# Kernel tuning notes

Measured on AMD Instinct MI355X. Metric: run time of the kernel, lower is better.

Reference implementation:

```python
import jax, jax.numpy as jnp
import numpy as np

EMBED = 1024
NUM_EXPERTS = 8
ACTIVE = 2
HIDDEN = 4 * EMBED


def setup_inputs() -> dict:
    key = jax.random.key(0)
    ks = jax.random.split(key, 7)
    B, T = 4, 1024
    s1 = 1.0 / np.sqrt(EMBED)
    s2 = 1.0 / np.sqrt(HIDDEN)
    return {
        "x": jax.random.normal(ks[0], (B, T, EMBED), dtype=jnp.float32),
        # stacked expert weights, layout [in, out] (torch Linear applies x @ W.T + b)
        "W1": jax.random.uniform(ks[1], (NUM_EXPERTS, EMBED, HIDDEN), jnp.float32, -s1, s1),
        "b1": jax.random.uniform(ks[2], (NUM_EXPERTS, HIDDEN), jnp.float32, -s1, s1),
        "W2": jax.random.uniform(ks[3], (NUM_EXPERTS, HIDDEN, EMBED), jnp.float32, -s2, s2),
        "b2": jax.random.uniform(ks[4], (NUM_EXPERTS, EMBED), jnp.float32, -s2, s2),
        "Wr": jax.random.uniform(ks[5], (EMBED, NUM_EXPERTS), jnp.float32, -s1, s1),
        "br": jax.random.uniform(ks[6], (NUM_EXPERTS,), jnp.float32, -s1, s1),
    }


def reference(x, W1, b1, W2, b2, Wr, br):
    # ---- router (TopkRouter) ----
    scores = x @ Wr + br                                  # [B,T,E]
    topk_scores, indices = jax.lax.top_k(scores, ACTIVE)  # [B,T,K]
    # mask = zeros scattered with topk scores at topk positions (others stay 0),
    # then softmax over ALL experts (faithful to the reference's quirky softmax).
    one_hot = jax.nn.one_hot(indices, NUM_EXPERTS, dtype=scores.dtype)  # [B,T,K,E]
    mask = jnp.einsum('btke,btk->bte', one_hot, topk_scores)            # [B,T,E]
    router_output = jax.nn.softmax(mask, axis=-1)                       # [B,T,E]

    # ---- dense all-experts FFN (Expert): relu(x@W1+b1)@W2+b2 per expert ----
    h = jax.nn.relu(jnp.einsum('btd,edh->bteh', x, W1) + b1)            # [B,T,E,H]
    expert_outputs = jnp.einsum('bteh,ehd->bted', h, W2) + b2           # [B,T,E,D]

    # ---- weighted combine ----
    return jnp.einsum('bte,bted->btd', router_output, expert_outputs)   # [B,T,D]
```

## Files before the change

### kernel.cpp

```cpp
#include <hip/hip_runtime.h>
#include <hip/hip_bf16.h>
#include <cstdint>
#include <cstddef>

#define EMBED  1024
#define NEXP   8
#define HIDDEN 4096
#define TOKENS 4096

typedef __attribute__((ext_vector_type(8))) short bf16x8;
typedef __attribute__((ext_vector_type(4))) float f32x4;
using bf16 = __hip_bfloat16;

__device__ __forceinline__ void gload_lds16(const void* g, void* l) {
    __builtin_amdgcn_global_load_lds((const __attribute__((address_space(1))) void*)g,
                                     (__attribute__((address_space(3))) void*)l,
                                     16, 0, 0);
}

__device__ __forceinline__ int swzB(int b) { return b ^ (((b >> 7) & 7) << 4); }

__global__ void cvt_kernel(const float* __restrict__ in, bf16* __restrict__ out, size_t n) {
    size_t i = ((size_t)blockIdx.x * blockDim.x + threadIdx.x) * 4;
    if (i + 3 < n) {
        float4 v = *(const float4*)(in + i);
        out[i + 0] = __float2bfloat16(v.x);
        out[i + 1] = __float2bfloat16(v.y);
        out[i + 2] = __float2bfloat16(v.z);
        out[i + 3] = __float2bfloat16(v.w);
    }
}

__global__ void transpose_cvt(const float* __restrict__ in, bf16* __restrict__ out,
                              int K, int N, size_t in_estride, size_t out_eoff, int ldo) {
    const int e = blockIdx.z;
    const float* ine = in + (size_t)e * in_estride;
    bf16* oute = out + (size_t)e * out_eoff;
    __shared__ float tile[32][33];
    const int n0 = blockIdx.x * 32, k0 = blockIdx.y * 32;
    const int tx = threadIdx.x, ty = threadIdx.y;
    #pragma unroll
    for (int i = ty; i < 32; i += 8)
        tile[i][tx] = ine[(size_t)(k0 + i) * N + n0 + tx];
    __syncthreads();
    #pragma unroll
    for (int i = ty; i < 32; i += 8)
        oute[(size_t)(n0 + i) * ldo + k0 + tx] = __float2bfloat16(tile[tx][i]);
}

__global__ void router_kernel(const float* __restrict__ x, const float* __restrict__ Wr,
                              const float* __restrict__ br, float* __restrict__ w) {
    const int t = blockIdx.x;
    const int lane = threadIdx.x;
    const float* xt = x + (size_t)t * EMBED;
    float s[NEXP];
    #pragma unroll
    for (int e = 0; e < NEXP; e++) s[e] = 0.f;
    for (int k = lane; k < EMBED; k += 64) {
        const float xv = xt[k];
        const float* wrk = Wr + (size_t)k * NEXP;
        #pragma unroll
        for (int e = 0; e < NEXP; e++) s[e] = fmaf(xv, wrk[e], s[e]);
    }
    #pragma unroll
    for (int e = 0; e < NEXP; e++) {
        #pragma unroll
        for (int off = 32; off >= 1; off >>= 1)
            s[e] += __shfl_xor(s[e], off);
    }
    if (lane == 0) {
        float sc[NEXP];
        #pragma unroll
        for (int e = 0; e < NEXP; e++) sc[e] = s[e] + br[e];
        int i1 = 0; float m1 = sc[0];
        #pragma unroll
        for (int e = 1; e < NEXP; e++) if (sc[e] > m1) { m1 = sc[e]; i1 = e; }
        int i2 = -1; float m2 = -1e30f;
        #pragma unroll
        for (int e = 0; e < NEXP; e++) if (e != i1 && sc[e] > m2) { m2 = sc[e]; i2 = e; }
        const float mx = fmaxf(m1, 0.f);
        const float denom = 6.f * expf(0.f - mx) + expf(m1 - mx) + expf(m2 - mx);
        #pragma unroll
        for (int e = 0; e < NEXP; e++) {
            float v = (e == i1) ? m1 : ((e == i2) ? m2 : 0.f);
            w[(size_t)t * NEXP + e] = expf(v - mx) / denom;
        }
    }
}

__global__ __launch_bounds__(256) void reduce_kernel(const float* __restrict__ p,
                                                     const float* __restrict__ rw,
                                                     const float* __restrict__ b2,
                                                     float* __restrict__ out) {
    const int row = blockIdx.x;
    const int c4 = threadIdx.x * 4;
    const size_t S = (size_t)TOKENS * EMBED;
    const float* pr = p + (size_t)row * EMBED + c4;
    float4 v0 = *(const float4*)(pr);
    float4 v1 = *(const float4*)(pr + S);
    float4 v2 = *(const float4*)(pr + 2 * S);
    float4 v3 = *(const float4*)(pr + 3 * S);
    float4 v;
    v.x = v0.x + v1.x + v2.x + v3.x;
    v.y = v0.y + v1.y + v2.y + v3.y;
    v.z = v0.z + v1.z + v2.z + v3.z;
    v.w = v0.w + v1.w + v2.w + v3.w;
    const float* wrow = rw + (size_t)row * NEXP;
    #pragma unroll
    for (int e = 0; e < NEXP; e++) {
        const float we = wrow[e];
        float4 bb = *(const float4*)(b2 + (size_t)e * EMBED + c4);
        v.x = fmaf(we, bb.x, v.x);
        v.y = fmaf(we, bb.y, v.y);
        v.z = fmaf(we, bb.z, v.z);
        v.w = fmaf(we, bb.w, v.w);
    }
    *(float4*)(out + (size_t)row * EMBED + c4) = v;
}

#define BARX()  { __builtin_amdgcn_sched_barrier(0); __builtin_amdgcn_s_barrier(); __builtin_amdgcn_sched_barrier(0); }
#define LGKM0() { asm volatile("s_waitcnt lgkmcnt(0)" ::: "memory"); __builtin_amdgcn_sched_barrier(0); }

#define KOFF(T, estride) ((size_t)((T) & 63) * 64 + (size_t)((T) >> 6) * (estride))

#define PIPE_PREAMBLE(Abase, Bbase, lda, ldb)                                        \
    __shared__ __align__(16) bf16 As[2][2][128 * 64];                                \
    __shared__ __align__(16) bf16 Bs[2][2][128 * 64];                                \
    const int tid = threadIdx.x;                                                     \
    const int lane = tid & 63, wid = tid >> 6;                                       \
    const int mhalf = wid >> 2, wB = wid & 3;                                        \
    const int nhalf = wB >> 1, nsub = wB & 1;                                        \
    const int wv_r = mhalf * 128, wv_c = wB * 64;                                    \
    f32x4 acc[8][4] = {};                                                            \
    int rowloc[2], colel[2];                                                         \
    _Pragma("unroll")                                                                \
    for (int j = 0; j < 2; j++) {                                                    \
        int bs = swzB(tid * 16 + j * 8192);                                          \
        rowloc[j] = bs >> 7; colel[j] = (bs & 127) >> 1;                             \
    }                                                                                \
    const bf16* pA0 = (Abase) + (size_t)(brow + rowloc[0]) * (lda) + colel[0];       \
    const bf16* pA1 = (Abase) + (size_t)(brow + rowloc[1]) * (lda) + colel[1];       \
    const bf16* pB0 = (Bbase) + (size_t)(bcol + rowloc[0]) * (ldb) + colel[0];       \
    const bf16* pB1 = (Bbase) + (size_t)(bcol + rowloc[1]) * (ldb) + colel[1];       \
    const int fr = lane & 15, kb0 = (lane >> 4) * 16;                                \
    const int xm = (fr & 7) << 4;                                                    \
    const int baA0 = (fr * 128 + kb0) ^ xm, baA1 = (fr * 128 + kb0 + 64) ^ xm;       \
    const int brB = (nsub * 64 + fr) * 128;                                          \
    const int baB0 = (brB + kb0) ^ xm, baB1 = (brB + kb0 + 64) ^ xm;

#define STAGE_A(bi, h, koff, lda)                                                    \
    do {                                                                             \
        gload_lds16(pA0 + (size_t)(h) * 128 * (lda) + (koff), &As[bi][h][tid * 8]);  \
        gload_lds16(pA1 + (size_t)(h) * 128 * (lda) + (koff), &As[bi][h][tid * 8 + 4096]); \
    } while (0)
#define STAGE_B(bi, h, koff, ldb)                                                    \
    do {                                                                             \
        gload_lds16(pB0 + (size_t)(h) * 128 * (ldb) + (koff), &Bs[bi][h][tid * 8]);  \
        gload_lds16(pB1 + (size_t)(h) * 128 * (ldb) + (koff), &Bs[bi][h][tid * 8 + 4096]); \
    } while (0)

#define MFMA_Q(mh, nh)                                                               \
    __builtin_amdgcn_s_setprio(1);                                                   \
    _Pragma("unroll")                                                                \
    for (int mm = 0; mm < 4; mm++)                                                   \
        _Pragma("unroll")                                                            \
        for (int nn = 0; nn < 2; nn++) {                                             \
            acc[(mh)*4+mm][(nh)*2+nn] = __builtin_amdgcn_mfma_f32_16x16x32_bf16(     \
                a[(mh)*4+mm][0], b[(nh)*2+nn][0], acc[(mh)*4+mm][(nh)*2+nn], 0,0,0); \
            acc[(mh)*4+mm][(nh)*2+nn] = __builtin_amdgcn_mfma_f32_16x16x32_bf16(     \
                a[(mh)*4+mm][1], b[(nh)*2+nn][1], acc[(mh)*4+mm][(nh)*2+nn], 0,0,0); \
        }                                                                            \
    __builtin_amdgcn_s_setprio(0);

#define PIPE_KLOOP(NT, lda, ldb, eA, eB)                                             \
    STAGE_A(0, 0, 0, lda); STAGE_A(0, 1, 0, lda);                                    \
    STAGE_B(0, 0, 0, ldb); STAGE_B(0, 1, 0, ldb);                                    \
    STAGE_A(1, 0, 64, lda); STAGE_A(1, 1, 64, lda);                                  \
    STAGE_B(1, 0, 64, ldb); STAGE_B(1, 1, 64, ldb);                                  \
    asm volatile("s_waitcnt vmcnt(8)" ::: "memory");                                 \
    BARX();                                                                          \
    for (int t = 0; t < (NT); ++t) {                                                 \
        const int bi = t & 1;                                                        \
        const bool st = (t + 2) < (NT);                                              \
        const size_t koffA = KOFF(t + 2, eA);                                        \
        const size_t koffB = KOFF(t + 2, eB);                                        \
        const char* Ah = (const char*)&As[bi][mhalf][0];                             \
        const char* Bh = (const char*)&Bs[bi][nhalf][0];                             \
        bf16x8 a[8][2], b[4][2];                                                     \
                                        \
        _Pragma("unroll")                                                            \
        for (int m = 0; m < 4; m++) {                                                \
            a[m][0] = *(const bf16x8*)(Ah + baA0 + m * 2048);                        \
            a[m][1] = *(const bf16x8*)(Ah + baA1 + m * 2048);                        \
        }                                                                            \
        _Pragma("unroll")                                                            \
        for (int n = 0; n < 2; n++) {                                                \
            b[n][0] = *(const bf16x8*)(Bh + baB0 + n * 2048);                        \
            b[n][1] = *(const bf16x8*)(Bh + baB1 + n * 2048);                        \
        }                                                                            \
        BARX(); LGKM0();                                                             \
        MFMA_Q(0, 0)                                                                 \
                                                   \
        _Pragma("unroll")                                                            \
        for (int n = 2; n < 4; n++) {                                                \
            b[n][0] = *(const bf16x8*)(Bh + baB0 + n * 2048);                        \
            b[n][1] = *(const bf16x8*)(Bh + baB1 + n * 2048);                        \
        }                                                                            \
        BARX(); LGKM0();                                                             \
        MFMA_Q(0, 1)                                                                 \
        BARX();                                                                      \
                                     \
        _Pragma("unroll")                                                            \
        for (int m = 4; m < 8; m++) {                                                \
            a[m][0] = *(const bf16x8*)(Ah + baA0 + m * 2048);                        \
            a[m][1] = *(const bf16x8*)(Ah + baA1 + m * 2048);                        \
        }                                                                            \
        if (st) { STAGE_B(bi, 0, koffB, ldb); STAGE_B(bi, 1, koffB, ldb); }          \
        BARX(); LGKM0();                                                             \
        MFMA_Q(1, 0)                                                                 \
        BARX();                                                                      \
                       \
        if (st) { STAGE_A(bi, 0, koffA, lda); STAGE_A(bi, 1, koffA, lda); }          \
        MFMA_Q(1, 1)                                                                 \
        if (st) { asm volatile("s_waitcnt vmcnt(8)" ::: "memory"); }                 \
        else    { asm volatile("s_waitcnt vmcnt(0)" ::: "memory"); }                 \
        BARX();                                                                      \
    }

__global__ __launch_bounds__(512, 2) void gemm1(const bf16* __restrict__ A,
                                                const bf16* __restrict__ Bt,
                                                const float* __restrict__ b1,
                                                const float* __restrict__ rw,
                                                bf16* __restrict__ H) {
    const int e = blockIdx.z;
    const int brow = blockIdx.y * 256;
    const int bcol = blockIdx.x * 256;
    const bf16* Be = Bt + (size_t)e * HIDDEN * EMBED;
    bf16* He = H + (size_t)e * TOKENS * HIDDEN;

    PIPE_PREAMBLE(A, Be, EMBED, EMBED)
    PIPE_KLOOP(16, EMBED, EMBED, (size_t)0, (size_t)0)

    #pragma unroll
    for (int n = 0; n < 4; n++) {
        const int col = bcol + wv_c + n * 16 + fr;
        const float bias = b1[e * HIDDEN + col];
        #pragma unroll
        for (int m = 0; m < 8; m++) {
            const int rowb = brow + wv_r + m * 16 + (lane >> 4) * 4;
            #pragma unroll
            for (int j = 0; j < 4; j++) {
                const int row = rowb + j;
                float v = acc[m][n][j] + bias;
                v = fmaxf(v, 0.f) * rw[(size_t)row * NEXP + e];
                He[(size_t)row * HIDDEN + col] = __float2bfloat16(v);
            }
        }
    }
}

__global__ __launch_bounds__(512, 2) void gemm2(const bf16* __restrict__ A,
                                                const bf16* __restrict__ Bt,
                                                float* __restrict__ partials) {
    const int kc = blockIdx.z;
    const int brow = blockIdx.y * 256;
    const int bcol = blockIdx.x * 256;
    const size_t eA = (size_t)TOKENS * HIDDEN;
    const size_t eB = (size_t)EMBED * HIDDEN;
    const bf16* Ae = A + (size_t)(kc * 2) * eA;
    const bf16* Be = Bt + (size_t)(kc * 2) * eB;
    float* pout = partials + (size_t)kc * TOKENS * EMBED;

    PIPE_PREAMBLE(Ae, Be, HIDDEN, HIDDEN)
    PIPE_KLOOP(128, HIDDEN, HIDDEN, eA, eB)

    #pragma unroll
    for (int n = 0; n < 4; n++) {
        const int col = bcol + wv_c + n * 16 + fr;
        #pragma unroll
        for (int m = 0; m < 8; m++) {
            const int rowb = brow + wv_r + m * 16 + (lane >> 4) * 4;
            #pragma unroll
            for (int j = 0; j < 4; j++) {
                const int row = rowb + j;
                pout[(size_t)row * EMBED + col] = acc[m][n][j];
            }
        }
    }
}

extern "C" void kernel_launch(void* const* d_in, const int* in_sizes, int n_in,
                              void* d_out, int out_size, void* d_ws, size_t ws_size,
                              hipStream_t stream) {
    const float* x  = (const float*)d_in[0];
    const float* W1 = (const float*)d_in[1];
    const float* b1 = (const float*)d_in[2];
    const float* W2 = (const float*)d_in[3];
    const float* b2 = (const float*)d_in[4];
    const float* Wr = (const float*)d_in[5];
    const float* br = (const float*)d_in[6];
    float* out = (float*)d_out;

    uint8_t* ws = (uint8_t*)d_ws;
    size_t off = 0;
    auto walloc = [&](size_t bytes) -> void* {
        void* p = ws + off;
        off += (bytes + 255) & ~(size_t)255;
        return p;
    };
    float* rw  = (float*)walloc((size_t)TOKENS * NEXP * 4);
    bf16* xb   = (bf16*)walloc((size_t)TOKENS * EMBED * 2);
    bf16* w1t  = (bf16*)walloc((size_t)NEXP * HIDDEN * EMBED * 2);
    bf16* w2t  = (bf16*)walloc((size_t)NEXP * EMBED * HIDDEN * 2);
    bf16* hbuf = (bf16*)walloc((size_t)NEXP * TOKENS * HIDDEN * 2);
    float* partials = (float*)w1t;

    cvt_kernel<<<4096, 256, 0, stream>>>(x, xb, (size_t)TOKENS * EMBED);

    dim3 tb(32, 8);
    transpose_cvt<<<dim3(HIDDEN / 32, EMBED / 32, NEXP), tb, 0, stream>>>(
        W1, w1t, EMBED, HIDDEN, (size_t)EMBED * HIDDEN, (size_t)HIDDEN * EMBED, EMBED);
    transpose_cvt<<<dim3(EMBED / 32, HIDDEN / 32, NEXP), tb, 0, stream>>>(
        W2, w2t, HIDDEN, EMBED, (size_t)HIDDEN * EMBED, (size_t)EMBED * HIDDEN, HIDDEN);

    router_kernel<<<TOKENS, 64, 0, stream>>>(x, Wr, br, rw);

    gemm1<<<dim3(HIDDEN / 256, TOKENS / 256, NEXP), 512, 0, stream>>>(xb, w1t, b1, rw, hbuf);
    gemm2<<<dim3(EMBED / 256, TOKENS / 256, 4), 512, 0, stream>>>(hbuf, w2t, partials);
    reduce_kernel<<<TOKENS, 256, 0, stream>>>(partials, rw, b2, out);
}
```

Before: 813.2 us.

## Make gemm1 persistent over eight row tiles with a continuous K pipeline

gemm1 now launches 256 blocks, each of which walks 8 consecutive 256-row tiles in a single 128-step pipelined loop. The loop keeps prefetching the next tile's A and B across tile boundaries, writes each tile's epilogue inline, and then zeroes the accumulators. Router weights and biases are staged into LDS and registers once per block, and the loop-body reads are factored into macros. The aim is to remove per-tile pipeline fill/drain and launch overhead. In exchange there are fewer blocks (256 on a large GPU), which risks under-occupancy, and the epilogue stores stall the pipeline.

```diff
diff --git a/kernel.cpp b/kernel.cpp
--- a/kernel.cpp
+++ b/kernel.cpp
@@ -172,6 +172,32 @@
         }                                                                            \
     __builtin_amdgcn_s_setprio(0);
 
+#define PH1_READS()                                                                  \
+    _Pragma("unroll")                                                                \
+    for (int m = 0; m < 4; m++) {                                                    \
+        a[m][0] = *(const bf16x8*)(Ah + baA0 + m * 2048);                            \
+        a[m][1] = *(const bf16x8*)(Ah + baA1 + m * 2048);                            \
+    }                                                                                \
+    _Pragma("unroll")                                                                \
+    for (int n = 0; n < 2; n++) {                                                    \
+        b[n][0] = *(const bf16x8*)(Bh + baB0 + n * 2048);                            \
+        b[n][1] = *(const bf16x8*)(Bh + baB1 + n * 2048);                            \
+    }
+
+#define PH2_READS()                                                                  \
+    _Pragma("unroll")                                                                \
+    for (int n = 2; n < 4; n++) {                                                    \
+        b[n][0] = *(const bf16x8*)(Bh + baB0 + n * 2048);                            \
+        b[n][1] = *(const bf16x8*)(Bh + baB1 + n * 2048);                            \
+    }
+
+#define PH3_READS()                                                                  \
+    _Pragma("unroll")                                                                \
+    for (int m = 4; m < 8; m++) {                                                    \
+        a[m][0] = *(const bf16x8*)(Ah + baA0 + m * 2048);                            \
+        a[m][1] = *(const bf16x8*)(Ah + baA1 + m * 2048);                            \
+    }
+
 #define PIPE_KLOOP(NT, lda, ldb, eA, eB)                                             \
     STAGE_A(0, 0, 0, lda); STAGE_A(0, 1, 0, lda);                                    \
     STAGE_B(0, 0, 0, ldb); STAGE_B(0, 1, 0, ldb);                                    \
@@ -187,39 +213,18 @@
         const char* Ah = (const char*)&As[bi][mhalf][0];                             \
         const char* Bh = (const char*)&Bs[bi][nhalf][0];                             \
         bf16x8 a[8][2], b[4][2];                                                     \
-                                        \
-        _Pragma("unroll")                                                            \
-        for (int m = 0; m < 4; m++) {                                                \
-            a[m][0] = *(const bf16x8*)(Ah + baA0 + m * 2048);                        \
-            a[m][1] = *(const bf16x8*)(Ah + baA1 + m * 2048);                        \
-        }                                                                            \
-        _Pragma("unroll")                                                            \
-        for (int n = 0; n < 2; n++) {                                                \
-            b[n][0] = *(const bf16x8*)(Bh + baB0 + n * 2048);                        \
-            b[n][1] = *(const bf16x8*)(Bh + baB1 + n * 2048);                        \
-        }                                                                            \
+        PH1_READS()                                                                  \
         BARX(); LGKM0();                                                             \
         MFMA_Q(0, 0)                                                                 \
-                                                   \
-        _Pragma("unroll")                                                            \
-        for (int n = 2; n < 4; n++) {                                                \
-            b[n][0] = *(const bf16x8*)(Bh + baB0 + n * 2048);                        \
-            b[n][1] = *(const bf16x8*)(Bh + baB1 + n * 2048);                        \
-        }                                                                            \
+        PH2_READS()                                                                  \
         BARX(); LGKM0();                                                             \
         MFMA_Q(0, 1)                                                                 \
         BARX();                                                                      \
-                                     \
-        _Pragma("unroll")                                                            \
-        for (int m = 4; m < 8; m++) {                                                \
-            a[m][0] = *(const bf16x8*)(Ah + baA0 + m * 2048);                        \
-            a[m][1] = *(const bf16x8*)(Ah + baA1 + m * 2048);                        \
-        }                                                                            \
+        PH3_READS()                                                                  \
         if (st) { STAGE_B(bi, 0, koffB, ldb); STAGE_B(bi, 1, koffB, ldb); }          \
         BARX(); LGKM0();                                                             \
         MFMA_Q(1, 0)                                                                 \
         BARX();                                                                      \
-                       \
         if (st) { STAGE_A(bi, 0, koffA, lda); STAGE_A(bi, 1, koffA, lda); }          \
         MFMA_Q(1, 1)                                                                 \
         if (st) { asm volatile("s_waitcnt vmcnt(8)" ::: "memory"); }                 \
@@ -233,29 +238,79 @@
                                                 const float* __restrict__ rw,
                                                 bf16* __restrict__ H) {
     const int e = blockIdx.z;
-    const int brow = blockIdx.y * 256;
     const int bcol = blockIdx.x * 256;
+    const int brow0 = blockIdx.y * 2048;
+    const int brow = brow0;
     const bf16* Be = Bt + (size_t)e * HIDDEN * EMBED;
     bf16* He = H + (size_t)e * TOKENS * HIDDEN;
 
     PIPE_PREAMBLE(A, Be, EMBED, EMBED)
-    PIPE_KLOOP(16, EMBED, EMBED, (size_t)0, (size_t)0)
-
-    #pragma unroll
-    for (int n = 0; n < 4; n++) {
-        const int col = bcol + wv_c + n * 16 + fr;
-        const float bias = b1[e * HIDDEN + col];
-        #pragma unroll
-        for (int m = 0; m < 8; m++) {
-            const int rowb = brow + wv_r + m * 16 + (lane >> 4) * 4;
+
+    __shared__ float rwLds[2048];
+    for (int i = tid; i < 2048; i += 512)
+        rwLds[i] = rw[(size_t)(brow0 + i) * NEXP + e];
+
+    float bias[4];
+    #pragma unroll
+    for (int n = 0; n < 4; n++) bias[n] = b1[e * HIDDEN + bcol + wv_c + n * 16 + fr];
+
+    __syncthreads();
+
+    STAGE_A(0, 0, 0, EMBED); STAGE_A(0, 1, 0, EMBED);
+    STAGE_B(0, 0, 0, EMBED); STAGE_B(0, 1, 0, EMBED);
+    STAGE_A(1, 0, 64, EMBED); STAGE_A(1, 1, 64, EMBED);
+    STAGE_B(1, 0, 64, EMBED); STAGE_B(1, 1, 64, EMBED);
+    asm volatile("s_waitcnt vmcnt(8)" ::: "memory");
+    BARX();
+
+    for (int t = 0; t < 128; ++t) {
+        const int bi = t & 1;
+        const bool st = (t + 2) < 128;
+        const int S = t + 2;
+        const size_t koffA = (size_t)(S >> 4) * (size_t)(256 * EMBED) + (size_t)(S & 15) * 64;
+        const size_t koffB = (size_t)(S & 15) * 64;
+        const char* Ah = (const char*)&As[bi][mhalf][0];
+        const char* Bh = (const char*)&Bs[bi][nhalf][0];
+        bf16x8 a[8][2], b[4][2];
+        PH1_READS()
+        BARX(); LGKM0();
+        MFMA_Q(0, 0)
+        PH2_READS()
+        BARX(); LGKM0();
+        MFMA_Q(0, 1)
+        BARX();
+        PH3_READS()
+        if (st) { STAGE_B(bi, 0, koffB, EMBED); STAGE_B(bi, 1, koffB, EMBED); }
+        BARX(); LGKM0();
+        MFMA_Q(1, 0)
+        BARX();
+        if (st) { STAGE_A(bi, 0, koffA, EMBED); STAGE_A(bi, 1, koffA, EMBED); }
+        MFMA_Q(1, 1)
+        if ((t & 15) == 15) {
+            const int rbase = (t >> 4) * 256 + wv_r;
             #pragma unroll
-            for (int j = 0; j < 4; j++) {
-                const int row = rowb + j;
-                float v = acc[m][n][j] + bias;
-                v = fmaxf(v, 0.f) * rw[(size_t)row * NEXP + e];
-                He[(size_t)row * HIDDEN + col] = __float2bfloat16(v);
+            for (int n = 0; n < 4; n++) {
+                const int col = bcol + wv_c + n * 16 + fr;
+                #pragma unroll
+                for (int m = 0; m < 8; m++) {
+                    const int rloc = rbase + m * 16 + (lane >> 4) * 4;
+                    #pragma unroll
+                    for (int j = 0; j < 4; j++) {
+                        float v = acc[m][n][j] + bias[n];
+                        v = fmaxf(v, 0.f) * rwLds[rloc + j];
+                        He[(size_t)(brow0 + rloc + j) * HIDDEN + col] = __float2bfloat16(v);
+                    }
+                }
             }
+            #pragma unroll
+            for (int m = 0; m < 8; m++)
+                #pragma unroll
+                for (int n = 0; n < 4; n++)
+                    acc[m][n] = (f32x4){0.f, 0.f, 0.f, 0.f};
         }
+        if (st) { asm volatile("s_waitcnt vmcnt(8)" ::: "memory"); }
+        else    { asm volatile("s_waitcnt vmcnt(0)" ::: "memory"); }
+        BARX();
     }
 }
 
@@ -325,7 +380,7 @@
 
     router_kernel<<<TOKENS, 64, 0, stream>>>(x, Wr, br, rw);
 
-    gemm1<<<dim3(HIDDEN / 256, TOKENS / 256, NEXP), 512, 0, stream>>>(xb, w1t, b1, rw, hbuf);
+    gemm1<<<dim3(16, 2, 8), 512, 0, stream>>>(xb, w1t, b1, rw, hbuf);
     gemm2<<<dim3(EMBED / 256, TOKENS / 256, 4), 512, 0, stream>>>(hbuf, w2t, partials);
     reduce_kernel<<<TOKENS, 256, 0, stream>>>(partials, rw, b2, out);
 }
```

Result: no change. 806.6 us (-0.8%).
